# Kernel optimization log

Measured on AMD Instinct MI355X. Metric: run time of the kernel, lower is better.

## Reference

```python
import jax, jax.numpy as jnp
import numpy as np
import math

B, L, H, NH = 4, 1024, 512, 8
D = H // NH

def setup_inputs() -> dict:
    key = jax.random.key(0)
    ks = jax.random.split(key, 12)
    s = 1.0 / math.sqrt(H)
    return {
        "key": jax.random.normal(ks[0], (B, L, H), jnp.float32),
        "query": jax.random.normal(ks[1], (B, L, H), jnp.float32),
        "value": jax.random.normal(ks[2], (B, L, H), jnp.float32),
        "rel_pos_embedding": jax.random.normal(ks[3], (B, NH, L, L), jnp.float32),
        "wk_w": jax.random.normal(ks[4], (H, H), jnp.float32) * s,
        "wk_b": jnp.zeros((H,), jnp.float32),
        "wq_w": jax.random.normal(ks[5], (H, H), jnp.float32) * s,
        "wq_b": jnp.zeros((H,), jnp.float32),
        "wv_w": jax.random.normal(ks[6], (H, H), jnp.float32) * s,
        "wv_b": jnp.zeros((H,), jnp.float32),
        "ff_w": jax.random.normal(ks[7], (H, H), jnp.float32) * s,
        "ff_b": jnp.zeros((H,), jnp.float32),
        "seq_len": jax.random.randint(ks[8], (B,), 1, 768, jnp.int32),
        "lex_num": jax.random.randint(ks[9], (B,), 0, 256, jnp.int32),
    }

def reference(key, query, value, rel_pos_embedding, wk_w, wk_b, wq_w, wq_b, wv_w, wv_b, ff_w, ff_b, seq_len, lex_num):
    b, l, h = key.shape
    # projections (torch Linear: x @ W^T + b)
    k = (key @ wk_w.T + wk_b).reshape(b, l, NH, D)
    q = (query @ wq_w.T + wq_b).reshape(b, l, NH, D)
    v = (value @ wv_w.T + wv_b).reshape(b, l, NH, D)
    # QK^T: [b, nh, lq, lk]
    scores = jnp.einsum("bqhd,bkhd->bhqk", q, k) / math.sqrt(D)
    scores = scores + rel_pos_embedding
    # padding mask over key positions
    lengths = (seq_len + lex_num).astype(jnp.int32)  # [b]
    mask = jnp.arange(l, dtype=jnp.int32)[None, :] < lengths[:, None]  # [b, l]
    scores = jnp.where(mask[:, None, None, :], scores, jnp.float32(-1e15))
    attn = jax.nn.softmax(scores, axis=-1)
    out = jnp.einsum("bhqk,bkhd->bqhd", attn, v).reshape(b, l, h)
    out = out @ ff_w.T + ff_b
    return out
```

## Files before the change

### kernel.cpp

```cpp
#include <hip/hip_runtime.h>
#include <hip/hip_bf16.h>

typedef __attribute__((ext_vector_type(8))) short bf16x8;
typedef __attribute__((ext_vector_type(4))) float f32x4;

__device__ __forceinline__ unsigned short f2bf(float f) {
    return __builtin_bit_cast(unsigned short, __float2bfloat16(f));
}

typedef const __attribute__((address_space(1))) void gvoid;
typedef __attribute__((address_space(3))) void lvoid;
#define GLDS(g, s) __builtin_amdgcn_global_load_lds((gvoid*)(g), (lvoid*)(s), 16, 0, 0)

__device__ __forceinline__ void block_barrier() {
    asm volatile("" ::: "memory");
    __builtin_amdgcn_s_barrier();
    asm volatile("" ::: "memory");
}

__global__ __launch_bounds__(256) void proj_kernel(
    const float* __restrict__ query, const float* __restrict__ key_, const float* __restrict__ value,
    const float* __restrict__ wq_w, const float* __restrict__ wq_b,
    const float* __restrict__ wk_w, const float* __restrict__ wk_b,
    const float* __restrict__ wv_w, const float* __restrict__ wv_b,
    unsigned short* __restrict__ Qb, unsigned short* __restrict__ Kb, unsigned short* __restrict__ Vt)
{
    const int wid = (blockIdx.x & 7) * 48 + (blockIdx.x >> 3);
    const int z = wid >> 7;
    const int rr = wid & 127;
    const int by = rr >> 2, bx = rr & 3;

    const float* X    = (z == 0) ? query : (z == 1) ? key_ : value;
    const float* W    = (z == 0) ? wq_w  : (z == 1) ? wk_w : wv_w;
    const float* bias = (z == 0) ? wq_b  : (z == 1) ? wk_b : wv_b;

    const int t = threadIdx.x;
    const int l = t & 63;
    const int w = t >> 6;
    const int wm = w >> 1, wn = w & 1;
    const int m0 = by * 128, n0 = bx * 128;

    __shared__ __align__(16) unsigned short As[128 * 32];
    __shared__ __align__(16) unsigned short Bs[128 * 32];

    f32x4 acc[4][4];
#pragma unroll
    for (int i = 0; i < 4; i++)
#pragma unroll
        for (int j = 0; j < 4; j++) acc[i][j] = (f32x4){0.f, 0.f, 0.f, 0.f};

    float4 ra[4], rb[4];
    auto LOAD = [&](int k0) {
#pragma unroll
        for (int i = 0; i < 4; i++) {
            int idx = t + 256 * i;
            int row = idx >> 3, c = idx & 7;
            ra[i] = *(const float4*)(X + (size_t)(m0 + row) * 512 + k0 + c * 4);
            rb[i] = *(const float4*)(W + (size_t)(n0 + row) * 512 + k0 + c * 4);
        }
    };
    LOAD(0);

    for (int k0 = 0; k0 < 512; k0 += 32) {
        if (k0) block_barrier();
#pragma unroll
        for (int i = 0; i < 4; i++) {
            int idx = t + 256 * i;
            int row = idx >> 3, c = idx & 7;
            __align__(8) unsigned short va[4] = {f2bf(ra[i].x), f2bf(ra[i].y), f2bf(ra[i].z), f2bf(ra[i].w)};
            *(uint2*)(As + row * 32 + (((c >> 1) ^ (row & 3)) * 8) + (c & 1) * 4) = *(uint2*)va;
            __align__(8) unsigned short vb[4] = {f2bf(rb[i].x), f2bf(rb[i].y), f2bf(rb[i].z), f2bf(rb[i].w)};
            *(uint2*)(Bs + row * 32 + (((c >> 1) ^ (row & 3)) * 8) + (c & 1) * 4) = *(uint2*)vb;
        }
        asm volatile("s_waitcnt lgkmcnt(0)" ::: "memory");
        block_barrier();
        if (k0 + 32 < 512) LOAD(k0 + 32);

        bf16x8 af[4], bfv[4];
#pragma unroll
        for (int mf = 0; mf < 4; mf++) {
            int row = wm * 64 + mf * 16 + (l & 15);
            af[mf] = *(const bf16x8*)(As + row * 32 + (((l >> 4) ^ (row & 3)) * 8));
        }
#pragma unroll
        for (int nf = 0; nf < 4; nf++) {
            int row = wn * 64 + nf * 16 + (l & 15);
            bfv[nf] = *(const bf16x8*)(Bs + row * 32 + (((l >> 4) ^ (row & 3)) * 8));
        }
#pragma unroll
        for (int mf = 0; mf < 4; mf++)
#pragma unroll
            for (int nf = 0; nf < 4; nf++)
                acc[mf][nf] = __builtin_amdgcn_mfma_f32_16x16x32_bf16(af[mf], bfv[nf], acc[mf][nf], 0, 0, 0);
    }

    if (z < 2) {
        unsigned short* dst = (z == 0) ? Qb : Kb;
#pragma unroll
        for (int nf = 0; nf < 4; nf++) {
            int n = n0 + wn * 64 + nf * 16 + (l & 15);
            float bv = bias[n];
            int h = n >> 6, d = n & 63;
#pragma unroll
            for (int mf = 0; mf < 4; mf++) {
                int mbase = m0 + wm * 64 + mf * 16 + 4 * (l >> 4);
                int bb = mbase >> 10;
#pragma unroll
                for (int r = 0; r < 4; r++) {
                    int lq = (mbase + r) & 1023;
                    dst[((size_t)(bb * 8 + h) * 1024 + lq) * 64 + d] = f2bf(acc[mf][nf][r] + bv);
                }
            }
        }
    } else {
#pragma unroll
        for (int nf = 0; nf < 4; nf++) {
            int n = n0 + wn * 64 + nf * 16 + (l & 15);
            float bv = bias[n];
            int h = n >> 6, d = n & 63;
#pragma unroll
            for (int mf = 0; mf < 4; mf++) {
                int mbase = m0 + wm * 64 + mf * 16 + 4 * (l >> 4);
                int bb = mbase >> 10;
                int lq0 = mbase & 1023;
                ushort4 pk;
                pk.x = f2bf(acc[mf][nf][0] + bv);
                pk.y = f2bf(acc[mf][nf][1] + bv);
                pk.z = f2bf(acc[mf][nf][2] + bv);
                pk.w = f2bf(acc[mf][nf][3] + bv);
                *(ushort4*)(Vt + ((size_t)(bb * 8 + h) * 64 + d) * 1024 + lq0) = pk;
            }
        }
    }
}

__global__ __launch_bounds__(256) void attn_kernel(
    const unsigned short* __restrict__ Qb, const unsigned short* __restrict__ Kb,
    const unsigned short* __restrict__ Vt, const float* __restrict__ rel_pos,
    const int* __restrict__ seq_len, const int* __restrict__ lex_num,
    unsigned short* __restrict__ AO)
{
    const int t = threadIdx.x;
    const int l = t & 63;
    const int w = t >> 6;
    const int wid = (blockIdx.x & 7) * 64 + (blockIdx.x >> 3);
    const int x8 = wid >> 6;
    const int g  = (wid >> 4) & 3;
    const int qt = wid & 15;
    const int b  = g;
    const int h  = (x8 + 2 * g) & 7;
    const int q0 = qt * 64;
    const int bh = b * 8 + h;
    const int len = seq_len[b] + lex_num[b];
    const int nkt = (len + 63) >> 6;

    __shared__ __align__(16) unsigned short Qs[64 * 64];
    __shared__ __align__(16) unsigned short Ks[2][64 * 64];
    __shared__ __align__(16) unsigned short Vs[2][64 * 64];
    __shared__ __align__(16) float Rs[2][64 * 64];
    __shared__ __align__(16) unsigned short Ps[4 * 16 * 64];

    const unsigned short* Qg = Qb + ((size_t)bh * 1024 + q0) * 64;
    const unsigned short* Kg = Kb + (size_t)bh * 1024 * 64;
    const unsigned short* Vg = Vt + (size_t)bh * 64 * 1024;
    const float* Rg = rel_pos + ((size_t)bh * 1024 + q0) * 1024;

    const int rl8 = l >> 3, c8 = l & 7;
    const int kvc = (c8 ^ rl8) * 8;
    const int rl16 = l >> 4, c16 = l & 15;

    auto STAGE = [&](int kt, int nb) {
        const int k0 = kt * 64;
#pragma unroll
        for (int j = 0; j < 2; j++) {
            int row = w * 16 + j * 8 + rl8;
            GLDS(Kg + (size_t)(k0 + row) * 64 + kvc, &Ks[nb][(w * 16 + j * 8) * 64]);
            GLDS(Vg + (size_t)row * 1024 + k0 + kvc, &Vs[nb][(w * 16 + j * 8) * 64]);
        }
#pragma unroll
        for (int j = 0; j < 4; j++) {
            int row = w * 16 + j * 4 + rl16;
            int cc = c16 ^ ((j * 4 + rl16) & 7);
            GLDS(Rg + (size_t)row * 1024 + k0 + cc * 4, &Rs[nb][(w * 16 + j * 4) * 64]);
        }
    };

    STAGE(0, 0);
#pragma unroll
    for (int j = 0; j < 2; j++) {
        int row = w * 16 + j * 8 + rl8;
        GLDS(Qg + (size_t)row * 64 + kvc, &Qs[(w * 16 + j * 8) * 64]);
    }
    asm volatile("s_waitcnt vmcnt(0)" ::: "memory");
    block_barrier();

    bf16x8 qf[2];
#pragma unroll
    for (int s = 0; s < 2; s++) {
        int row = w * 16 + (l & 15);
        int ch = 4 * s + (l >> 4);
        qf[s] = *(const bf16x8*)(Qs + row * 64 + ((ch ^ (row & 7)) * 8));
    }

    f32x4 oacc[4];
#pragma unroll
    for (int dn = 0; dn < 4; dn++) oacc[dn] = (f32x4){0.f, 0.f, 0.f, 0.f};
    float m_run[4] = {-3.0e38f, -3.0e38f, -3.0e38f, -3.0e38f};
    float l_run[4] = {0.f, 0.f, 0.f, 0.f};

    unsigned short* Pw = Ps + w * 1024;

    for (int kt = 0; kt < nkt; kt++) {
        const int cur = kt & 1;
        const int k0 = kt * 64;
        if (kt + 1 < nkt) {
            STAGE(kt + 1, cur ^ 1);
            asm volatile("s_waitcnt vmcnt(8)" ::: "memory");
        } else {
            asm volatile("s_waitcnt vmcnt(0)" ::: "memory");
        }
        block_barrier();

        const unsigned short* Ksc = Ks[cur];
        const unsigned short* Vsc = Vs[cur];
        const float* Rsc = Rs[cur];

        float rel[4][4];
#pragma unroll
        for (int kn = 0; kn < 4; kn++) {
            int ccb = kn * 4 + ((l >> 2) & 3);
#pragma unroll
            for (int r = 0; r < 4; r++) {
                int qrow = 4 * (l >> 4) + r;
                rel[kn][r] = Rsc[(w * 16 + qrow) * 64 + ((ccb ^ (qrow & 7)) * 4) + (l & 3)];
            }
        }

        f32x4 sa[4];
#pragma unroll
        for (int kn = 0; kn < 4; kn++) sa[kn] = (f32x4){0.f, 0.f, 0.f, 0.f};
        __builtin_amdgcn_s_setprio(1);
#pragma unroll
        for (int s = 0; s < 2; s++)
#pragma unroll
            for (int kn = 0; kn < 4; kn++) {
                int krow = kn * 16 + (l & 15);
                int ch = 4 * s + (l >> 4);
                bf16x8 kf = *(const bf16x8*)(Ksc + krow * 64 + ((ch ^ (krow & 7)) * 8));
                sa[kn] = __builtin_amdgcn_mfma_f32_16x16x32_bf16(qf[s], kf, sa[kn], 0, 0, 0);
            }
        __builtin_amdgcn_s_setprio(0);

        float p[4][4];
#pragma unroll
        for (int r = 0; r < 4; r++) {
            float sv[4];
#pragma unroll
            for (int kn = 0; kn < 4; kn++) {
                int kg = k0 + kn * 16 + (l & 15);
                float x = sa[kn][r] * 0.125f + rel[kn][r];
                sv[kn] = (kg < len) ? x : -1e15f;
            }
            float mx = fmaxf(fmaxf(sv[0], sv[1]), fmaxf(sv[2], sv[3]));
#pragma unroll
            for (int o = 1; o < 16; o <<= 1) mx = fmaxf(mx, __shfl_xor(mx, o, 64));
            float mn = fmaxf(m_run[r], mx);
            float scale = __expf(m_run[r] - mn);
            m_run[r] = mn;
            float rs = 0.f;
#pragma unroll
            for (int kn = 0; kn < 4; kn++) { p[kn][r] = __expf(sv[kn] - mn); rs += p[kn][r]; }
#pragma unroll
            for (int o = 1; o < 16; o <<= 1) rs += __shfl_xor(rs, o, 64);
            l_run[r] = l_run[r] * scale + rs;
#pragma unroll
            for (int dn = 0; dn < 4; dn++) oacc[dn][r] *= scale;
        }

#pragma unroll
        for (int kn = 0; kn < 4; kn++)
#pragma unroll
            for (int r = 0; r < 4; r++) {
                int qrow = 4 * (l >> 4) + r;
                int k = kn * 16 + (l & 15);
                Pw[qrow * 64 + (((k >> 3) ^ (qrow & 7)) * 8) + (k & 7)] = f2bf(p[kn][r]);
            }

        __builtin_amdgcn_s_setprio(1);
#pragma unroll
        for (int s = 0; s < 2; s++) {
            int arow = (l & 15);
            bf16x8 pf = *(const bf16x8*)(Pw + arow * 64 + (((4 * s + (l >> 4)) ^ (arow & 7)) * 8));
#pragma unroll
            for (int dn = 0; dn < 4; dn++) {
                int drow = dn * 16 + (l & 15);
                bf16x8 vf = *(const bf16x8*)(Vsc + drow * 64 + (((4 * s + (l >> 4)) ^ (drow & 7)) * 8));
                oacc[dn] = __builtin_amdgcn_mfma_f32_16x16x32_bf16(pf, vf, oacc[dn], 0, 0, 0);
            }
        }
        __builtin_amdgcn_s_setprio(0);
        block_barrier();
    }

    unsigned short* AOg = AO + ((size_t)(b * 1024 + q0 + w * 16)) * 512 + h * 64;
#pragma unroll
    for (int r = 0; r < 4; r++) {
        float inv = 1.0f / l_run[r];
        int qrow = 4 * (l >> 4) + r;
#pragma unroll
        for (int dn = 0; dn < 4; dn++)
            AOg[(size_t)qrow * 512 + dn * 16 + (l & 15)] = f2bf(oacc[dn][r] * inv);
    }
}

__global__ __launch_bounds__(256) void ff_kernel(
    const unsigned short* __restrict__ AO, const float* __restrict__ ff_w,
    const float* __restrict__ ff_b, float* __restrict__ out)
{
    const int t = threadIdx.x;
    const int l = t & 63;
    const int w = t >> 6;
    const int wm = w >> 1, wn = w & 1;
    const int wid = (blockIdx.x & 7) * 32 + (blockIdx.x >> 3);
    const int by = wid >> 2;
    const int bx = wid & 3;
    const int m0 = by * 64, n0 = bx * 128;

    __shared__ __align__(16) unsigned short As[64 * 32];
    __shared__ __align__(16) unsigned short Bs[128 * 32];

    f32x4 acc[2][4];
#pragma unroll
    for (int i = 0; i < 2; i++)
#pragma unroll
        for (int j = 0; j < 4; j++) acc[i][j] = (f32x4){0.f, 0.f, 0.f, 0.f};

    uint4 ua;
    float4 rbf[4];
    const int arow = t >> 2, ac = t & 3;
    auto LOAD = [&](int k0) {
        ua = *(const uint4*)(AO + (size_t)(m0 + arow) * 512 + k0 + ac * 8);
#pragma unroll
        for (int i = 0; i < 4; i++) {
            int idx = t + 256 * i;
            int row = idx >> 3, c = idx & 7;
            rbf[i] = *(const float4*)(ff_w + (size_t)(n0 + row) * 512 + k0 + c * 4);
        }
    };
    LOAD(0);

    for (int k0 = 0; k0 < 512; k0 += 32) {
        if (k0) block_barrier();
        *(uint4*)(As + arow * 32 + ((ac ^ (arow & 3)) * 8)) = ua;
#pragma unroll
        for (int i = 0; i < 4; i++) {
            int idx = t + 256 * i;
            int row = idx >> 3, c = idx & 7;
            __align__(8) unsigned short vb[4] = {f2bf(rbf[i].x), f2bf(rbf[i].y), f2bf(rbf[i].z), f2bf(rbf[i].w)};
            *(uint2*)(Bs + row * 32 + (((c >> 1) ^ (row & 3)) * 8) + (c & 1) * 4) = *(uint2*)vb;
        }
        asm volatile("s_waitcnt lgkmcnt(0)" ::: "memory");
        block_barrier();
        if (k0 + 32 < 512) LOAD(k0 + 32);

        bf16x8 af[2], bfv[4];
#pragma unroll
        for (int mf = 0; mf < 2; mf++) {
            int row = wm * 32 + mf * 16 + (l & 15);
            af[mf] = *(const bf16x8*)(As + row * 32 + (((l >> 4) ^ (row & 3)) * 8));
        }
#pragma unroll
        for (int nf = 0; nf < 4; nf++) {
            int row = wn * 64 + nf * 16 + (l & 15);
            bfv[nf] = *(const bf16x8*)(Bs + row * 32 + (((l >> 4) ^ (row & 3)) * 8));
        }
#pragma unroll
        for (int mf = 0; mf < 2; mf++)
#pragma unroll
            for (int nf = 0; nf < 4; nf++)
                acc[mf][nf] = __builtin_amdgcn_mfma_f32_16x16x32_bf16(af[mf], bfv[nf], acc[mf][nf], 0, 0, 0);
    }

#pragma unroll
    for (int nf = 0; nf < 4; nf++) {
        int n = n0 + wn * 64 + nf * 16 + (l & 15);
        float bv = ff_b[n];
#pragma unroll
        for (int mf = 0; mf < 2; mf++) {
            int mbase = m0 + wm * 32 + mf * 16 + 4 * (l >> 4);
#pragma unroll
            for (int r = 0; r < 4; r++)
                out[(size_t)(mbase + r) * 512 + n] = acc[mf][nf][r] + bv;
        }
    }
}

extern "C" void kernel_launch(void* const* d_in, const int* in_sizes, int n_in,
                              void* d_out, int out_size, void* d_ws, size_t ws_size,
                              hipStream_t stream) {
    const float* key   = (const float*)d_in[0];
    const float* query = (const float*)d_in[1];
    const float* value = (const float*)d_in[2];
    const float* rel   = (const float*)d_in[3];
    const float* wk_w  = (const float*)d_in[4];
    const float* wk_b  = (const float*)d_in[5];
    const float* wq_w  = (const float*)d_in[6];
    const float* wq_b  = (const float*)d_in[7];
    const float* wv_w  = (const float*)d_in[8];
    const float* wv_b  = (const float*)d_in[9];
    const float* ff_w  = (const float*)d_in[10];
    const float* ff_b  = (const float*)d_in[11];
    const int* seq_len = (const int*)d_in[12];
    const int* lex_num = (const int*)d_in[13];
    float* out = (float*)d_out;

    unsigned short* Qb = (unsigned short*)d_ws;
    unsigned short* Kb = Qb + 2097152;
    unsigned short* Vt = Kb + 2097152;
    unsigned short* AO = Vt + 2097152;

    proj_kernel<<<dim3(384), 256, 0, stream>>>(query, key, value,
                                               wq_w, wq_b, wk_w, wk_b, wv_w, wv_b,
                                               Qb, Kb, Vt);
    attn_kernel<<<dim3(512), 256, 0, stream>>>(Qb, Kb, Vt, rel, seq_len, lex_num, AO);
    ff_kernel<<<dim3(256), 256, 0, stream>>>(AO, ff_w, ff_b, out);
}
```

Before: 69.68 us.

## Load rel_pos directly into registers with double-buffering, drop LDS staging

The rel_pos tile is no longer staged through LDS via global_load_lds. Each lane now loads its own rel_pos values straight into registers, using two register arrays that alternate across a 2x-unrolled key-tile loop so the next tile's values are prefetched. This frees 32KB of LDS and adds an occupancy hint of 3 blocks per CU, aiming for more resident waves. In exchange the register loads are 4-byte accesses strided across rows, less coalesced than before, and they add register pressure.

After: 69.96 us. Within noise of the previous version (+0.4%).

```diff
diff --git a/kernel.cpp b/kernel.cpp
--- a/kernel.cpp
+++ b/kernel.cpp
@@ -134,7 +134,7 @@
     }
 }
 
-__global__ __launch_bounds__(256) void attn_kernel(
+__global__ __launch_bounds__(256, 3) void attn_kernel(
     const unsigned short* __restrict__ Qb, const unsigned short* __restrict__ Kb,
     const unsigned short* __restrict__ Vt, const float* __restrict__ rel_pos,
     const int* __restrict__ seq_len, const int* __restrict__ lex_num,
@@ -157,7 +157,6 @@
     __shared__ __align__(16) unsigned short Qs[64 * 64];
     __shared__ __align__(16) unsigned short Ks[2][64 * 64];
     __shared__ __align__(16) unsigned short Vs[2][64 * 64];
-    __shared__ __align__(16) float Rs[2][64 * 64];
     __shared__ __align__(16) unsigned short Ps[4 * 16 * 64];
 
     const unsigned short* Qg = Qb + ((size_t)bh * 1024 + q0) * 64;
@@ -167,74 +166,65 @@
 
     const int rl8 = l >> 3, c8 = l & 7;
     const int kvc = (c8 ^ rl8) * 8;
-    const int rl16 = l >> 4, c16 = l & 15;
-
-    auto STAGE = [&](int kt, int nb) {
-        const int k0 = kt * 64;
+
+    auto STAGE_KV = [&](int kt2, int nb) {
+        const int k0s = kt2 * 64;
 #pragma unroll
         for (int j = 0; j < 2; j++) {
             int row = w * 16 + j * 8 + rl8;
-            GLDS(Kg + (size_t)(k0 + row) * 64 + kvc, &Ks[nb][(w * 16 + j * 8) * 64]);
-            GLDS(Vg + (size_t)row * 1024 + k0 + kvc, &Vs[nb][(w * 16 + j * 8) * 64]);
-        }
-#pragma unroll
-        for (int j = 0; j < 4; j++) {
-            int row = w * 16 + j * 4 + rl16;
-            int cc = c16 ^ ((j * 4 + rl16) & 7);
-            GLDS(Rg + (size_t)row * 1024 + k0 + cc * 4, &Rs[nb][(w * 16 + j * 4) * 64]);
+            GLDS(Kg + (size_t)(k0s + row) * 64 + kvc, &Ks[nb][(w * 16 + j * 8) * 64]);
+            GLDS(Vg + (size_t)row * 1024 + k0s + kvc, &Vs[nb][(w * 16 + j * 8) * 64]);
         }
     };
-
-    STAGE(0, 0);
+    auto RELLOAD = [&](float (&R)[16], int kt2) {
+        const float* rp = Rg + (size_t)(w * 16 + 4 * (l >> 4)) * 1024 + kt2 * 64 + (l & 15);
+#pragma unroll
+        for (int r = 0; r < 4; r++)
+#pragma unroll
+            for (int kn = 0; kn < 4; kn++)
+                R[4 * r + kn] = rp[(size_t)r * 1024 + kn * 16];
+    };
+
+    float rA[16], rB[16];
 #pragma unroll
     for (int j = 0; j < 2; j++) {
         int row = w * 16 + j * 8 + rl8;
         GLDS(Qg + (size_t)row * 64 + kvc, &Qs[(w * 16 + j * 8) * 64]);
     }
-    asm volatile("s_waitcnt vmcnt(0)" ::: "memory");
-    block_barrier();
+    STAGE_KV(0, 0);
+    RELLOAD(rA, 0);
 
     bf16x8 qf[2];
-#pragma unroll
-    for (int s = 0; s < 2; s++) {
-        int row = w * 16 + (l & 15);
-        int ch = 4 * s + (l >> 4);
-        qf[s] = *(const bf16x8*)(Qs + row * 64 + ((ch ^ (row & 7)) * 8));
-    }
-
     f32x4 oacc[4];
 #pragma unroll
     for (int dn = 0; dn < 4; dn++) oacc[dn] = (f32x4){0.f, 0.f, 0.f, 0.f};
     float m_run[4] = {-3.0e38f, -3.0e38f, -3.0e38f, -3.0e38f};
     float l_run[4] = {0.f, 0.f, 0.f, 0.f};
-
     unsigned short* Pw = Ps + w * 1024;
 
-    for (int kt = 0; kt < nkt; kt++) {
+    auto tile_body = [&](int kt, float (&REL)[16], float (&RELN)[16]) {
         const int cur = kt & 1;
         const int k0 = kt * 64;
         if (kt + 1 < nkt) {
-            STAGE(kt + 1, cur ^ 1);
-            asm volatile("s_waitcnt vmcnt(8)" ::: "memory");
+            STAGE_KV(kt + 1, cur ^ 1);
+            RELLOAD(RELN, kt + 1);
+            asm volatile("s_waitcnt vmcnt(20)" ::: "memory");
         } else {
             asm volatile("s_waitcnt vmcnt(0)" ::: "memory");
         }
         block_barrier();
 
+        if (kt == 0) {
+#pragma unroll
+            for (int s = 0; s < 2; s++) {
+                int row = w * 16 + (l & 15);
+                int ch = 4 * s + (l >> 4);
+                qf[s] = *(const bf16x8*)(Qs + row * 64 + ((ch ^ (row & 7)) * 8));
+            }
+        }
+
         const unsigned short* Ksc = Ks[cur];
         const unsigned short* Vsc = Vs[cur];
-        const float* Rsc = Rs[cur];
-
-        float rel[4][4];
-#pragma unroll
-        for (int kn = 0; kn < 4; kn++) {
-            int ccb = kn * 4 + ((l >> 2) & 3);
-#pragma unroll
-            for (int r = 0; r < 4; r++) {
-                int qrow = 4 * (l >> 4) + r;
-                rel[kn][r] = Rsc[(w * 16 + qrow) * 64 + ((ccb ^ (qrow & 7)) * 4) + (l & 3)];
-            }
-        }
 
         f32x4 sa[4];
 #pragma unroll
@@ -258,7 +248,7 @@
 #pragma unroll
             for (int kn = 0; kn < 4; kn++) {
                 int kg = k0 + kn * 16 + (l & 15);
-                float x = sa[kn][r] * 0.125f + rel[kn][r];
+                float x = sa[kn][r] * 0.125f + REL[4 * r + kn];
                 sv[kn] = (kg < len) ? x : -1e15f;
             }
             float mx = fmaxf(fmaxf(sv[0], sv[1]), fmaxf(sv[2], sv[3]));
@@ -300,6 +290,11 @@
         }
         __builtin_amdgcn_s_setprio(0);
         block_barrier();
+    };
+
+    for (int kt = 0; kt < nkt; kt += 2) {
+        tile_body(kt, rA, rB);
+        if (kt + 1 < nkt) tile_body(kt + 1, rB, rA);
     }
 
     unsigned short* AOg = AO + ((size_t)(b * 1024 + q0 + w * 16)) * 512 + h * 64;
```
